# Kernel optimization log

Hardware: AMD Instinct MI355X
Metric: run time of the kernel (lower is better)

## Reference

```python
import jax, jax.numpy as jnp
import numpy as np

N_HEAD = 4
N_FEAT = 256
D_K = N_FEAT // N_HEAD


def setup_inputs() -> dict:
    key = jax.random.key(0)
    ks = jax.random.split(key, 7)
    B, T, F = 8, 2048, N_FEAT
    return {
        "query": jax.random.normal(ks[0], (B, T, F), dtype=jnp.float32),
        "key": jax.random.normal(ks[1], (B, T, F), dtype=jnp.float32),
        "value": jax.random.normal(ks[2], (B, T, F), dtype=jnp.float32),
        "mask": jax.random.randint(ks[3], (B, 1, T), 0, 2, dtype=jnp.int32),
        "W_qkv": jax.random.normal(ks[4], (3 * F, 3 * F), dtype=jnp.float32) * 0.02,
        "b_qkv": jnp.zeros((3 * F,), dtype=jnp.float32),
        "W_out": jax.random.normal(ks[5], (F, F), dtype=jnp.float32) * 0.02,
        "b_out": jnp.zeros((F,), dtype=jnp.float32),
    }


def reference(query, key, value, mask, W_qkv, b_qkv, W_out, b_out):
    B, T, F = query.shape
    H, dk = N_HEAD, D_K
    # fused QKV projection on concatenated [q; k; v]  -> (B, T, 3F)
    qkv = jnp.concatenate([query, key, value], axis=-1) @ W_qkv.T + b_qkv
    qkv = qkv.reshape(B, T, H, 3 * dk)
    q, k, v = jnp.split(qkv, 3, axis=-1)          # each (B, T, H, dk)
    q = q.transpose(0, 2, 1, 3)                    # (B, H, T, dk)
    k = k.transpose(0, 2, 1, 3)
    v = v.transpose(0, 2, 1, 3)
    scores = jnp.einsum("bhqd,bhkd->bhqk", q, k) / jnp.sqrt(jnp.float32(dk))
    # mask: (B, 1, T) -> broadcast (B, 1, 1, T); positions where mask==0 are masked
    m = (mask[:, None, :, :] == 0)
    min_val = jnp.finfo(scores.dtype).min
    scores = jnp.where(m, min_val, scores)
    attn = jax.nn.softmax(scores, axis=-1)
    attn = jnp.where(m, jnp.float32(0.0), attn)    # zero masked probs, as in torch code
    x = jnp.einsum("bhqk,bhkd->bhqd", attn, v)     # (B, H, T, dk)
    x = x.transpose(0, 2, 1, 3).reshape(B, T, H * dk)
    return x @ W_out.T + b_out
```

## Files before the change

### kernel.cpp

```cpp
#include <hip/hip_runtime.h>
#include <hip/hip_bf16.h>

#define NB 8
#define NT 2048
#define NH 4
#define NF 256
#define NTF 768
#define NM (NB * NT)

typedef unsigned short u16;
typedef unsigned int u32;
typedef unsigned long long u64;
typedef u16 u16x8 __attribute__((ext_vector_type(8)));
typedef __bf16 bf16x8 __attribute__((ext_vector_type(8)));
typedef float f32x4 __attribute__((ext_vector_type(4)));
typedef float f32x16 __attribute__((ext_vector_type(16)));

__device__ __forceinline__ u16 bf16_rne(float f) {
    union { float f; unsigned u; } x; x.f = f;
    unsigned u = x.u;
    return (u16)((u + 0x7fffu + ((u >> 16) & 1u)) >> 16);
}

__device__ __forceinline__ int swz(int row, int colB) {
    return row * 128 + (colB ^ ((row & 7) << 4));
}

__device__ __forceinline__ void glds16(const void* g, void* l) {
    __builtin_amdgcn_global_load_lds(
        (const __attribute__((address_space(1))) void*)g,
        (__attribute__((address_space(3))) void*)l, 16, 0, 0);
}

__device__ __forceinline__ u32 pkbf16(float lo, float hi) {
    union { __bf16 h2[2]; u32 u; } t;
    t.h2[0] = (__bf16)lo; t.h2[1] = (__bf16)hi;
    return t.u;
}

__device__ __forceinline__ void pl32swap(u32& a, u32& b) {
    asm("v_permlane32_swap_b32 %0, %1" : "+v"(a), "+v"(b));
}

#define mfma16(A, B, C) __builtin_amdgcn_mfma_f32_16x16x32_bf16((A), (B), (C), 0, 0, 0)
#define mfma32(A, B, C) __builtin_amdgcn_mfma_f32_32x32x16_bf16((A), (B), (C), 0, 0, 0)

__global__ __launch_bounds__(256) void convert_all_kernel(
        const float* __restrict__ q, const float* __restrict__ k,
        const float* __restrict__ v, const float* __restrict__ wqkv,
        const float* __restrict__ wout, const int* __restrict__ mask,
        u16* __restrict__ xcat, u16* __restrict__ wqkvb,
        u16* __restrict__ woutb, float* __restrict__ maskadd) {
    int bid = blockIdx.x;
    if (bid < 6144) {
        int tid = bid * 256 + threadIdx.x;
        int row = tid / 96;
        int c8  = (tid % 96) * 8;
        const float* src; int c;
        if (c8 < NF)            { src = q; c = c8; }
        else if (c8 < 2 * NF)   { src = k; c = c8 - NF; }
        else                    { src = v; c = c8 - 2 * NF; }
        const float4* p = reinterpret_cast<const float4*>(src + (size_t)row * NF + c);
        float4 a = p[0], b = p[1];
        u16x8 o;
        o[0] = bf16_rne(a.x); o[1] = bf16_rne(a.y); o[2] = bf16_rne(a.z); o[3] = bf16_rne(a.w);
        o[4] = bf16_rne(b.x); o[5] = bf16_rne(b.y); o[6] = bf16_rne(b.z); o[7] = bf16_rne(b.w);
        *reinterpret_cast<u16x8*>(xcat + (size_t)row * NTF + c8) = o;
    } else if (bid < 6464) {
        int tid = (bid - 6144) * 256 + threadIdx.x;
        int i8 = tid * 8;
        const float* src; u16* dst; int off;
        if (i8 < NTF * NTF) { src = wqkv; dst = wqkvb; off = i8; }
        else                { src = wout; dst = woutb; off = i8 - NTF * NTF; }
        const float4* p = reinterpret_cast<const float4*>(src + off);
        float4 a = p[0], b = p[1];
        u16x8 o;
        o[0] = bf16_rne(a.x); o[1] = bf16_rne(a.y); o[2] = bf16_rne(a.z); o[3] = bf16_rne(a.w);
        o[4] = bf16_rne(b.x); o[5] = bf16_rne(b.y); o[6] = bf16_rne(b.z); o[7] = bf16_rne(b.w);
        *reinterpret_cast<u16x8*>(dst + off) = o;
    } else {
        int i = (bid - 6464) * 2048 + threadIdx.x * 8;
        int4 m0 = *reinterpret_cast<const int4*>(mask + i);
        int4 m1 = *reinterpret_cast<const int4*>(mask + i + 4);
        float4 f0 = { m0.x ? 0.f : -1e30f, m0.y ? 0.f : -1e30f,
                      m0.z ? 0.f : -1e30f, m0.w ? 0.f : -1e30f };
        float4 f1 = { m1.x ? 0.f : -1e30f, m1.y ? 0.f : -1e30f,
                      m1.z ? 0.f : -1e30f, m1.w ? 0.f : -1e30f };
        *reinterpret_cast<float4*>(maskadd + i) = f0;
        *reinterpret_cast<float4*>(maskadd + i + 4) = f1;
    }
}

template<int N, int K, int MODE>
__global__ __launch_bounds__(256) void gemm128_kernel(
        const u16* __restrict__ A, const u16* __restrict__ Bw,
        const float* __restrict__ bias, void* __restrict__ Cout,
        u16* __restrict__ Vt) {
    __shared__ alignas(16) char smem[65536];
    char* As = smem;
    char* Bs = smem + 32768;
    int m0 = blockIdx.x * 128, n0 = blockIdx.y * 128;
    int tid = threadIdx.x;
    int w = tid >> 6, lane = tid & 63, l15 = lane & 15, hi = lane >> 4;
    int wr = w >> 1, wc = w & 1;
    int r0 = tid >> 3, cb0 = (tid & 7) * 16;
    int gcb = cb0 ^ ((r0 & 7) << 4);
    int wo = w * 1024;

    const char* Ac = (const char*)A;
    const char* Bc = (const char*)Bw;
    const char* gA = Ac + (size_t)(m0 + r0) * (K * 2) + gcb;
    const char* gB = Bc + (size_t)(n0 + r0) * (K * 2) + gcb;
    const size_t rstep = (size_t)32 * (K * 2);

#pragma unroll
    for (int p = 0; p < 4; ++p) {
        glds16(gA + p * rstep, As + p * 4096 + wo);
        glds16(gB + p * rstep, Bs + p * 4096 + wo);
    }

    f32x4 acc[4][4];
#pragma unroll
    for (int fi = 0; fi < 4; ++fi)
#pragma unroll
        for (int fj = 0; fj < 4; ++fj) acc[fi][fj] = (f32x4){0.f, 0.f, 0.f, 0.f};

    constexpr int NKT = K / 64;
    for (int kt = 0; kt < NKT; ++kt) {
        int cur = kt & 1;
        __syncthreads();
        if (kt + 1 < NKT) {
            int off = (kt + 1) * 128;
            char* Ad = As + (cur ^ 1) * 16384;
            char* Bd = Bs + (cur ^ 1) * 16384;
#pragma unroll
            for (int p = 0; p < 4; ++p) {
                glds16(gA + p * rstep + off, Ad + p * 4096 + wo);
                glds16(gB + p * rstep + off, Bd + p * 4096 + wo);
            }
        }
        const char* Ax = As + cur * 16384;
        const char* Bx = Bs + cur * 16384;
#pragma unroll
        for (int ks = 0; ks < 2; ++ks) {
            bf16x8 af[4], bf[4];
#pragma unroll
            for (int fi = 0; fi < 4; ++fi)
                af[fi] = *reinterpret_cast<const bf16x8*>(
                    Ax + swz(wr * 64 + fi * 16 + l15, hi * 16 + ks * 64));
#pragma unroll
            for (int fj = 0; fj < 4; ++fj)
                bf[fj] = *reinterpret_cast<const bf16x8*>(
                    Bx + swz(wc * 64 + fj * 16 + l15, hi * 16 + ks * 64));
#pragma unroll
            for (int fi = 0; fi < 4; ++fi)
#pragma unroll
                for (int fj = 0; fj < 4; ++fj)
                    acc[fi][fj] = mfma16(af[fi], bf[fj], acc[fi][fj]);
        }
    }

    int rowBase = m0 + wr * 64;
    if constexpr (MODE == 2) {
        int g64 = (n0 >> 6) + wc;
        int typ = g64 % 3, h = g64 / 3;
        if (typ == 2) {
            int b = rowBase >> 11;
            int bh = b * NH + h;
#pragma unroll
            for (int fi = 0; fi < 4; ++fi) {
                int t = (rowBase + fi * 16 + hi * 4) & (NT - 1);
#pragma unroll
                for (int fj = 0; fj < 4; ++fj) {
                    int d = fj * 16 + l15;
                    float bv = bias[n0 + wc * 64 + d];
                    u32 lo = pkbf16(acc[fi][fj][0] + bv, acc[fi][fj][1] + bv);
                    u32 hi2 = pkbf16(acc[fi][fj][2] + bv, acc[fi][fj][3] + bv);
                    u64 pk = (u64)lo | ((u64)hi2 << 32);
                    *reinterpret_cast<u64*>(Vt + (size_t)(bh * 64 + d) * NT + t) = pk;
                }
            }
        } else {
#pragma unroll
            for (int fi = 0; fi < 4; ++fi) {
                int orow = rowBase + fi * 16 + hi * 4;
#pragma unroll
                for (int fj = 0; fj < 4; ++fj) {
                    int col = n0 + wc * 64 + fj * 16 + l15;
                    float bv = bias[col];
#pragma unroll
                    for (int r = 0; r < 4; ++r)
                        reinterpret_cast<u16*>(Cout)[(size_t)(orow + r) * N + col] =
                            bf16_rne(acc[fi][fj][r] + bv);
                }
            }
        }
    } else {
#pragma unroll
        for (int fi = 0; fi < 4; ++fi) {
            int orow = rowBase + fi * 16 + hi * 4;
#pragma unroll
            for (int fj = 0; fj < 4; ++fj) {
                int col = n0 + wc * 64 + fj * 16 + l15;
                float bv = bias[col];
#pragma unroll
                for (int r = 0; r < 4; ++r)
                    reinterpret_cast<float*>(Cout)[(size_t)(orow + r) * N + col] =
                        acc[fi][fj][r] + bv;
            }
        }
    }
}

__global__ __launch_bounds__(256, 4) void attn_kernel(
        const u16* __restrict__ qkv, const u16* __restrict__ vt,
        const float* __restrict__ maskadd, u16* __restrict__ xout) {
    int bh = blockIdx.x;
    int q0 = blockIdx.y * 128;
    int b = bh >> 2, h = bh & 3;
    __shared__ alignas(16) char smem[32768];
    int tid = threadIdx.x;
    int w = tid >> 6, lane = tid & 63;
    int l31 = lane & 31, hv = lane >> 5;
    int r0 = tid >> 3, cb0 = (tid & 7) * 16;
    int gcb = cb0 ^ ((r0 & 7) << 4);
    int wo = w * 1024;
    const float SCALE = 0.125f * 1.44269504088896340736f;

    const char* qkvC = (const char*)qkv;
    const char* vtC  = (const char*)vt;
    const char* gk0 = qkvC + (size_t)(b * NT + r0) * 1536 + h * 384 + 128 + gcb;
    const char* gv0 = vtC + (size_t)(bh * 64 + r0) * (NT * 2) + gcb;
    const float* gm = maskadd + (size_t)b * NT;

    glds16(gk0,              smem + wo);
    glds16(gk0 + 32 * 1536,  smem + 4096 + wo);
    glds16(gv0,              smem + 16384 + wo);
    glds16(gv0 + 32 * 4096,  smem + 16384 + 4096 + wo);

    const char* qrow = qkvC + (size_t)(b * NT + q0 + w * 32 + l31) * 1536
                       + h * 384 + hv * 16;
    bf16x8 bQ0 = *reinterpret_cast<const bf16x8*>(qrow);
    bf16x8 bQ1 = *reinterpret_cast<const bf16x8*>(qrow + 32);
    bf16x8 bQ2 = *reinterpret_cast<const bf16x8*>(qrow + 64);
    bf16x8 bQ3 = *reinterpret_cast<const bf16x8*>(qrow + 96);

    f32x16 accO0 = 0.f, accO1 = 0.f;
    float ssum = 0.f;

    for (int j = 0; j < NT / 64; ++j) {
        int cur = j & 1;
        __syncthreads();
        if (j < NT / 64 - 1) {
            char* Kd = smem + (cur ^ 1) * 8192;
            char* Vd = smem + 16384 + (cur ^ 1) * 8192;
            size_t ko = (size_t)(j + 1) * 98304;
            size_t vo2 = (size_t)(j + 1) * 128;
            glds16(gk0 + ko,             Kd + wo);
            glds16(gk0 + ko + 32 * 1536, Kd + 4096 + wo);
            glds16(gv0 + vo2,            Vd + wo);
            glds16(gv0 + vo2 + 32 * 4096, Vd + 4096 + wo);
        }
        const char* Kx = smem + cur * 8192;
        const char* Vx = smem + 16384 + cur * 8192;
        const float* mt = gm + j * 64;

#pragma unroll
        for (int kb = 0; kb < 2; ++kb) {
            f32x16 s = 0.f;
            __builtin_amdgcn_s_setprio(1);
#pragma unroll
            for (int ks = 0; ks < 4; ++ks) {
                bf16x8 a = *reinterpret_cast<const bf16x8*>(
                    Kx + swz(kb * 32 + l31, ks * 32 + hv * 16));
                bf16x8 bq = (ks == 0) ? bQ0 : (ks == 1) ? bQ1 : (ks == 2) ? bQ2 : bQ3;
                s = mfma32(a, bq, s);
            }
            __builtin_amdgcn_s_setprio(0);

#pragma unroll
            for (int rq = 0; rq < 4; ++rq) {
                f32x4 md = *reinterpret_cast<const f32x4*>(mt + kb * 32 + rq * 8 + 4 * hv);
#pragma unroll
                for (int e = 0; e < 4; ++e)
                    s[rq * 4 + e] = __builtin_amdgcn_exp2f(
                        __builtin_fmaf(s[rq * 4 + e], SCALE, md[e]));
            }
            {
                union { f32x16 v; f32x4 q[4]; } u; u.v = s;
                f32x4 r4 = (u.q[0] + u.q[1]) + (u.q[2] + u.q[3]);
                ssum += (r4[0] + r4[1]) + (r4[2] + r4[3]);
            }
            u32 pa[4], pb[4];
#pragma unroll
            for (int rq = 0; rq < 4; ++rq) {
                pa[rq] = pkbf16(s[rq * 4 + 0], s[rq * 4 + 1]);
                pb[rq] = pkbf16(s[rq * 4 + 2], s[rq * 4 + 3]);
            }
            __builtin_amdgcn_s_setprio(1);
#pragma unroll
            for (int sp2 = 0; sp2 < 2; ++sp2) {
                const int sp = sp2 * 2;
                u32 B0 = pa[sp], B2 = pa[sp + 1], B1 = pb[sp], B3 = pb[sp + 1];
                pl32swap(B0, B2);
                pl32swap(B1, B3);
                union { u32 u4[4]; bf16x8 v; } bp;
                bp.u4[0] = B0; bp.u4[1] = B1; bp.u4[2] = B2; bp.u4[3] = B3;
                int s4 = 2 * kb + sp2;
                bf16x8 av0 = *reinterpret_cast<const bf16x8*>(
                    Vx + swz(l31, s4 * 32 + hv * 16));
                bf16x8 av1 = *reinterpret_cast<const bf16x8*>(
                    Vx + swz(32 + l31, s4 * 32 + hv * 16));
                accO0 = mfma32(av0, bp.v, accO0);
                accO1 = mfma32(av1, bp.v, accO1);
            }
            __builtin_amdgcn_s_setprio(0);
        }
    }

    ssum += __shfl_xor(ssum, 32, 64);
    float inv = ssum > 0.f ? 1.0f / ssum : 0.0f;
    int qg = b * NT + q0 + w * 32 + l31;
    union { f32x16 v; float f[16]; } o0, o1; o0.v = accO0; o1.v = accO1;
#pragma unroll
    for (int db = 0; db < 2; ++db) {
        const float* of = db ? o1.f : o0.f;
#pragma unroll
        for (int rq = 0; rq < 4; ++rq) {
            u32 lo = pkbf16(of[rq * 4 + 0] * inv, of[rq * 4 + 1] * inv);
            u32 hi2 = pkbf16(of[rq * 4 + 2] * inv, of[rq * 4 + 3] * inv);
            u64 pk = (u64)lo | ((u64)hi2 << 32);
            int d = db * 32 + rq * 8 + 4 * hv;
            *reinterpret_cast<u64*>(xout + (size_t)qg * NF + h * 64 + d) = pk;
        }
    }
}

extern "C" void kernel_launch(void* const* d_in, const int* in_sizes, int n_in,
                              void* d_out, int out_size, void* d_ws, size_t ws_size,
                              hipStream_t stream) {
    const float* q    = (const float*)d_in[0];
    const float* k    = (const float*)d_in[1];
    const float* v    = (const float*)d_in[2];
    const int*   mask = (const int*)d_in[3];
    const float* wqkv = (const float*)d_in[4];
    const float* bqkv = (const float*)d_in[5];
    const float* wout = (const float*)d_in[6];
    const float* bout = (const float*)d_in[7];
    float* out = (float*)d_out;

    char* ws = (char*)d_ws;
    u16*   Xcat    = (u16*)(ws);
    u16*   QKV     = (u16*)(ws + 25165824);
    u16*   Vt      = (u16*)(ws + 50331648);
    u16*   Xattn   = (u16*)(ws + 58720256);
    u16*   Wqkvb   = (u16*)(ws + 67108864);
    u16*   Woutb   = (u16*)(ws + 68288512);
    float* Maskadd = (float*)(ws + 68419584);

    convert_all_kernel<<<6472, 256, 0, stream>>>(q, k, v, wqkv, wout, mask,
                                                 Xcat, Wqkvb, Woutb, Maskadd);
    gemm128_kernel<NTF, NTF, 2><<<dim3(NM / 128, NTF / 128), 256, 0, stream>>>(
        Xcat, Wqkvb, bqkv, QKV, Vt);
    attn_kernel<<<dim3(NB * NH, NT / 128), 256, 0, stream>>>(QKV, Vt, Maskadd, Xattn);
    gemm128_kernel<NF, NF, 1><<<dim3(NM / 128, NF / 128), 256, 0, stream>>>(
        Xattn, Woutb, bout, out, nullptr);
}
```

Before: 110.8 us.

## Split attention key dimension across wave pairs with 64-query blocks

Each attention block now covers 64 queries instead of 128. The four waves form two groups, and each group handles half of every 64-key tile. The partial output accumulators and row sums are then combined through shared memory before normalization. This doubles the grid to 1024 blocks for better occupancy and load balance across CUs. The cost is that K and V tiles are loaded twice as often per query, and the end adds an LDS reduction with extra barriers.

Result: faster. 105.1 us (-5.2%).

```diff
diff --git a/kernel.cpp b/kernel.cpp
--- a/kernel.cpp
+++ b/kernel.cpp
@@ -216,12 +216,13 @@
         const u16* __restrict__ qkv, const u16* __restrict__ vt,
         const float* __restrict__ maskadd, u16* __restrict__ xout) {
     int bh = blockIdx.x;
-    int q0 = blockIdx.y * 128;
+    int q0 = blockIdx.y * 64;
     int b = bh >> 2, h = bh & 3;
     __shared__ alignas(16) char smem[32768];
     int tid = threadIdx.x;
     int w = tid >> 6, lane = tid & 63;
     int l31 = lane & 31, hv = lane >> 5;
+    int wq = w & 1, g = w >> 1;
     int r0 = tid >> 3, cb0 = (tid & 7) * 16;
     int gcb = cb0 ^ ((r0 & 7) << 4);
     int wo = w * 1024;
@@ -238,7 +239,7 @@
     glds16(gv0,              smem + 16384 + wo);
     glds16(gv0 + 32 * 4096,  smem + 16384 + 4096 + wo);
 
-    const char* qrow = qkvC + (size_t)(b * NT + q0 + w * 32 + l31) * 1536
+    const char* qrow = qkvC + (size_t)(b * NT + q0 + wq * 32 + l31) * 1536
                        + h * 384 + hv * 16;
     bf16x8 bQ0 = *reinterpret_cast<const bf16x8*>(qrow);
     bf16x8 bQ1 = *reinterpret_cast<const bf16x8*>(qrow + 32);
@@ -256,82 +257,101 @@
             char* Vd = smem + 16384 + (cur ^ 1) * 8192;
             size_t ko = (size_t)(j + 1) * 98304;
             size_t vo2 = (size_t)(j + 1) * 128;
-            glds16(gk0 + ko,             Kd + wo);
-            glds16(gk0 + ko + 32 * 1536, Kd + 4096 + wo);
-            glds16(gv0 + vo2,            Vd + wo);
+            glds16(gk0 + ko,              Kd + wo);
+            glds16(gk0 + ko + 32 * 1536,  Kd + 4096 + wo);
+            glds16(gv0 + vo2,             Vd + wo);
             glds16(gv0 + vo2 + 32 * 4096, Vd + 4096 + wo);
         }
         const char* Kx = smem + cur * 8192;
         const char* Vx = smem + 16384 + cur * 8192;
         const float* mt = gm + j * 64;
 
-#pragma unroll
-        for (int kb = 0; kb < 2; ++kb) {
-            f32x16 s = 0.f;
-            __builtin_amdgcn_s_setprio(1);
-#pragma unroll
-            for (int ks = 0; ks < 4; ++ks) {
-                bf16x8 a = *reinterpret_cast<const bf16x8*>(
-                    Kx + swz(kb * 32 + l31, ks * 32 + hv * 16));
-                bf16x8 bq = (ks == 0) ? bQ0 : (ks == 1) ? bQ1 : (ks == 2) ? bQ2 : bQ3;
-                s = mfma32(a, bq, s);
-            }
-            __builtin_amdgcn_s_setprio(0);
-
+        f32x16 s = 0.f;
+        __builtin_amdgcn_s_setprio(1);
+#pragma unroll
+        for (int ks = 0; ks < 4; ++ks) {
+            bf16x8 a = *reinterpret_cast<const bf16x8*>(
+                Kx + swz(g * 32 + l31, ks * 32 + hv * 16));
+            bf16x8 bq = (ks == 0) ? bQ0 : (ks == 1) ? bQ1 : (ks == 2) ? bQ2 : bQ3;
+            s = mfma32(a, bq, s);
+        }
+        __builtin_amdgcn_s_setprio(0);
+
+#pragma unroll
+        for (int rq = 0; rq < 4; ++rq) {
+            f32x4 md = *reinterpret_cast<const f32x4*>(mt + g * 32 + rq * 8 + 4 * hv);
+#pragma unroll
+            for (int e = 0; e < 4; ++e)
+                s[rq * 4 + e] = __builtin_amdgcn_exp2f(
+                    __builtin_fmaf(s[rq * 4 + e], SCALE, md[e]));
+        }
+        {
+            union { f32x16 v; f32x4 q[4]; } u; u.v = s;
+            f32x4 r4 = (u.q[0] + u.q[1]) + (u.q[2] + u.q[3]);
+            ssum += (r4[0] + r4[1]) + (r4[2] + r4[3]);
+        }
+        u32 pa[4], pb[4];
+#pragma unroll
+        for (int rq = 0; rq < 4; ++rq) {
+            pa[rq] = pkbf16(s[rq * 4 + 0], s[rq * 4 + 1]);
+            pb[rq] = pkbf16(s[rq * 4 + 2], s[rq * 4 + 3]);
+        }
+        __builtin_amdgcn_s_setprio(1);
+#pragma unroll
+        for (int sp2 = 0; sp2 < 2; ++sp2) {
+            const int sp = sp2 * 2;
+            u32 B0 = pa[sp], B2 = pa[sp + 1], B1 = pb[sp], B3 = pb[sp + 1];
+            pl32swap(B0, B2);
+            pl32swap(B1, B3);
+            union { u32 u4[4]; bf16x8 v; } bp;
+            bp.u4[0] = B0; bp.u4[1] = B1; bp.u4[2] = B2; bp.u4[3] = B3;
+            int s4 = 2 * g + sp2;
+            bf16x8 av0 = *reinterpret_cast<const bf16x8*>(
+                Vx + swz(l31, s4 * 32 + hv * 16));
+            bf16x8 av1 = *reinterpret_cast<const bf16x8*>(
+                Vx + swz(32 + l31, s4 * 32 + hv * 16));
+            accO0 = mfma32(av0, bp.v, accO0);
+            accO1 = mfma32(av1, bp.v, accO1);
+        }
+        __builtin_amdgcn_s_setprio(0);
+    }
+
+    ssum += __shfl_xor(ssum, 32, 64);
+    __syncthreads();
+    float* sS = reinterpret_cast<float*>(smem + 16384);
+    if (g == 1) {
+        union { f32x16 v; f32x4 q[4]; } o0, o1; o0.v = accO0; o1.v = accO1;
+#pragma unroll
+        for (int i = 0; i < 4; ++i) {
+            *reinterpret_cast<f32x4*>(smem + wq * 8192 + i * 1024 + lane * 16) = o0.q[i];
+            *reinterpret_cast<f32x4*>(smem + wq * 8192 + (4 + i) * 1024 + lane * 16) = o1.q[i];
+        }
+        if (lane < 32) sS[wq * 32 + l31] = ssum;
+    }
+    __syncthreads();
+    if (g == 0) {
+        union { f32x16 v; f32x4 q[4]; } o0, o1; o0.v = accO0; o1.v = accO1;
+#pragma unroll
+        for (int i = 0; i < 4; ++i) {
+            o0.q[i] += *reinterpret_cast<const f32x4*>(smem + wq * 8192 + i * 1024 + lane * 16);
+            o1.q[i] += *reinterpret_cast<const f32x4*>(smem + wq * 8192 + (4 + i) * 1024 + lane * 16);
+        }
+        float stot = ssum + sS[wq * 32 + l31];
+        float inv = stot > 0.f ? 1.0f / stot : 0.0f;
+        int qg = b * NT + q0 + wq * 32 + l31;
+        const float* of0 = (const float*)&o0.v;
+        const float* of1 = (const float*)&o1.v;
+#pragma unroll
+        for (int db = 0; db < 2; ++db) {
+            const float* of = db ? of1 : of0;
 #pragma unroll
             for (int rq = 0; rq < 4; ++rq) {
-                f32x4 md = *reinterpret_cast<const f32x4*>(mt + kb * 32 + rq * 8 + 4 * hv);
-#pragma unroll
-                for (int e = 0; e < 4; ++e)
-                    s[rq * 4 + e] = __builtin_amdgcn_exp2f(
-                        __builtin_fmaf(s[rq * 4 + e], SCALE, md[e]));
-            }
-            {
-                union { f32x16 v; f32x4 q[4]; } u; u.v = s;
-                f32x4 r4 = (u.q[0] + u.q[1]) + (u.q[2] + u.q[3]);
-                ssum += (r4[0] + r4[1]) + (r4[2] + r4[3]);
-            }
-            u32 pa[4], pb[4];
-#pragma unroll
-            for (int rq = 0; rq < 4; ++rq) {
-                pa[rq] = pkbf16(s[rq * 4 + 0], s[rq * 4 + 1]);
-                pb[rq] = pkbf16(s[rq * 4 + 2], s[rq * 4 + 3]);
-            }
-            __builtin_amdgcn_s_setprio(1);
-#pragma unroll
-            for (int sp2 = 0; sp2 < 2; ++sp2) {
-                const int sp = sp2 * 2;
-                u32 B0 = pa[sp], B2 = pa[sp + 1], B1 = pb[sp], B3 = pb[sp + 1];
-                pl32swap(B0, B2);
-                pl32swap(B1, B3);
-                union { u32 u4[4]; bf16x8 v; } bp;
-                bp.u4[0] = B0; bp.u4[1] = B1; bp.u4[2] = B2; bp.u4[3] = B3;
-                int s4 = 2 * kb + sp2;
-                bf16x8 av0 = *reinterpret_cast<const bf16x8*>(
-                    Vx + swz(l31, s4 * 32 + hv * 16));
-                bf16x8 av1 = *reinterpret_cast<const bf16x8*>(
-                    Vx + swz(32 + l31, s4 * 32 + hv * 16));
-                accO0 = mfma32(av0, bp.v, accO0);
-                accO1 = mfma32(av1, bp.v, accO1);
-            }
-            __builtin_amdgcn_s_setprio(0);
-        }
-    }
-
-    ssum += __shfl_xor(ssum, 32, 64);
-    float inv = ssum > 0.f ? 1.0f / ssum : 0.0f;
-    int qg = b * NT + q0 + w * 32 + l31;
-    union { f32x16 v; float f[16]; } o0, o1; o0.v = accO0; o1.v = accO1;
-#pragma unroll
-    for (int db = 0; db < 2; ++db) {
-        const float* of = db ? o1.f : o0.f;
-#pragma unroll
-        for (int rq = 0; rq < 4; ++rq) {
-            u32 lo = pkbf16(of[rq * 4 + 0] * inv, of[rq * 4 + 1] * inv);
-            u32 hi2 = pkbf16(of[rq * 4 + 2] * inv, of[rq * 4 + 3] * inv);
-            u64 pk = (u64)lo | ((u64)hi2 << 32);
-            int d = db * 32 + rq * 8 + 4 * hv;
-            *reinterpret_cast<u64*>(xout + (size_t)qg * NF + h * 64 + d) = pk;
+                u32 lo = pkbf16(of[rq * 4 + 0] * inv, of[rq * 4 + 1] * inv);
+                u32 hi2 = pkbf16(of[rq * 4 + 2] * inv, of[rq * 4 + 3] * inv);
+                u64 pk = (u64)lo | ((u64)hi2 << 32);
+                int d = db * 32 + rq * 8 + 4 * hv;
+                *reinterpret_cast<u64*>(xout + (size_t)qg * NF + h * 64 + d) = pk;
+            }
         }
     }
 }
@@ -362,7 +382,7 @@
                                                  Xcat, Wqkvb, Woutb, Maskadd);
     gemm128_kernel<NTF, NTF, 2><<<dim3(NM / 128, NTF / 128), 256, 0, stream>>>(
         Xcat, Wqkvb, bqkv, QKV, Vt);
-    attn_kernel<<<dim3(NB * NH, NT / 128), 256, 0, stream>>>(QKV, Vt, Maskadd, Xattn);
+    attn_kernel<<<dim3(NB * NH, NT / 64), 256, 0, stream>>>(QKV, Vt, Maskadd, Xattn);
     gemm128_kernel<NF, NF, 1><<<dim3(NM / 128, NF / 128), 256, 0, stream>>>(
         Xattn, Woutb, bout, out, nullptr);
 }
```
